# Kernel tuning notes

Hardware: AMD Instinct MI355X
Metric: run time of the kernel (lower is better)

The kernel has to match this reference:

```python
import jax, jax.numpy as jnp
import numpy as np
from math import sqrt


def setup_inputs() -> dict:
    key0 = jax.random.key(0)
    ks = jax.random.split(key0, 7)
    N, H, E, D, S = 32, 16, 128, 128, 2047
    return {
        "query": jax.random.normal(ks[0], (N, H, E), dtype=jnp.float32),
        "key": jax.random.normal(ks[1], (N, H, E), dtype=jnp.float32),
        "value": jax.random.normal(ks[2], (N, H, D), dtype=jnp.float32),
        "keys_cache": jax.random.normal(ks[3], (N, H, S, E), dtype=jnp.float32),
        "values_cache": jax.random.normal(ks[4], (N, H, S, D), dtype=jnp.float32),
        "w_pre": jax.random.normal(ks[5], (H, H), dtype=jnp.float32) * (1.0 / sqrt(H)),
        "w_post": jax.random.normal(ks[6], (H, H), dtype=jnp.float32) * (1.0 / sqrt(H)),
    }


def reference(query, key, value, keys_cache, values_cache, w_pre, w_post):
    # Single recurrent decode step with talking-heads mixing (dropout in eval mode).
    N, H, E = query.shape
    softmax_temp = 1.0 / sqrt(E)
    # Append current key/value to the cache: [N,H,S+1,E] / [N,H,S+1,D]
    keys = jnp.concatenate([keys_cache, key[:, :, None, :]], axis=2)
    values = jnp.concatenate([values_cache, value[:, :, None, :]], axis=2)
    # Scores: [N,H,S]
    QK = jnp.einsum('nhe,nhse->nhs', query, keys)
    # Pre-softmax talking heads (1x1 conv over head axis): out_g = sum_h w[g,h] * in_h
    QK = jnp.einsum('gh,nhs->ngs', w_pre, QK)
    A = jax.nn.softmax(softmax_temp * QK, axis=-1)
    # Post-softmax talking heads
    A = jnp.einsum('gh,nhs->ngs', w_post, A)
    # Weighted value readout: [N,H,D]
    V = jnp.einsum('nhs,nhsd->nhd', A, values)
    return V, keys, values
```

## Files before the change

### kernel.cpp

```cpp
#include <hip/hip_runtime.h>
#include <cstddef>

constexpr int N_  = 32;
constexpr int H_  = 16;
constexpr int E_  = 128;
constexpr int D_  = 128;
constexpr int S_  = 2047;
constexpr int SP1 = 2048;
constexpr int NH  = N_ * H_;

constexpr int ROWS_PER_BLOCK = 256;
constexpr int CHUNKS = SP1 / ROWS_PER_BLOCK;

typedef float vfloat4 __attribute__((ext_vector_type(4)));

__global__ __launch_bounds__(256) void k1_keys_scores(
    const float* __restrict__ query, const float* __restrict__ key,
    const float* __restrict__ keys_cache,
    float* __restrict__ keys_out, float* __restrict__ scores)
{
  __shared__ float sc[ROWS_PER_BLOCK];
  const int bid   = blockIdx.x;
  const int nh    = bid / CHUNKS;
  const int chunk = bid % CHUNKS;
  const int tid   = threadIdx.x;
  const int wave  = tid >> 6;
  const int lane  = tid & 63;
  const int half  = lane >> 5;
  const int lcol  = lane & 31;

  const vfloat4 q4 = *reinterpret_cast<const vfloat4*>(query + (size_t)nh * E_ + lcol * 4);

  #pragma unroll 8
  for (int it = 0; it < ROWS_PER_BLOCK / 8; ++it) {
    const int r = it * 8 + wave * 2 + half;
    const int s = chunk * ROWS_PER_BLOCK + r;
    const float* src = (s < S_) ? (keys_cache + ((size_t)nh * S_ + s) * E_)
                                : (key + (size_t)nh * E_);
    vfloat4 k4 = *reinterpret_cast<const vfloat4*>(src + lcol * 4);
    __builtin_nontemporal_store(k4,
        reinterpret_cast<vfloat4*>(keys_out + ((size_t)nh * SP1 + s) * E_ + lcol * 4));

    float p = q4.x * k4.x + q4.y * k4.y + q4.z * k4.z + q4.w * k4.w;
    p += __shfl_xor(p, 1);
    p += __shfl_xor(p, 2);
    p += __shfl_xor(p, 4);
    p += __shfl_xor(p, 8);
    p += __shfl_xor(p, 16);
    if (lcol == 0) sc[r] = p;
  }
  __syncthreads();
  scores[(size_t)nh * SP1 + chunk * ROWS_PER_BLOCK + tid] = sc[tid];
}

__global__ __launch_bounds__(512) void k2_mix_softmax(
    const float* __restrict__ w_pre, const float* __restrict__ scores,
    float* __restrict__ a_out)
{
  __shared__ float wl[H_];
  __shared__ float redmax[8];
  __shared__ float redsum[8];
  const int n = blockIdx.x >> 4;
  const int g = blockIdx.x & 15;
  const int tid = threadIdx.x;
  const int wave = tid >> 6;
  const int lane = tid & 63;
  const float temp = 0.08838834764831845f;

  if (tid < H_) wl[tid] = w_pre[g * H_ + tid];
  __syncthreads();

  const float* base = scores + (size_t)n * H_ * SP1 + tid * 4;
  float a0 = 0.0f, a1 = 0.0f, a2 = 0.0f, a3 = 0.0f;
  #pragma unroll
  for (int h = 0; h < H_; ++h) {
    vfloat4 v = *reinterpret_cast<const vfloat4*>(base + (size_t)h * SP1);
    const float w = wl[h];
    a0 += w * v.x; a1 += w * v.y; a2 += w * v.z; a3 += w * v.w;
  }
  a0 *= temp; a1 *= temp; a2 *= temp; a3 *= temp;

  float lmax = fmaxf(fmaxf(a0, a1), fmaxf(a2, a3));
  #pragma unroll
  for (int m = 1; m <= 32; m <<= 1) lmax = fmaxf(lmax, __shfl_xor(lmax, m));
  if (lane == 0) redmax[wave] = lmax;
  __syncthreads();
  float bmax = redmax[0];
  #pragma unroll
  for (int w = 1; w < 8; ++w) bmax = fmaxf(bmax, redmax[w]);

  a0 = __expf(a0 - bmax); a1 = __expf(a1 - bmax);
  a2 = __expf(a2 - bmax); a3 = __expf(a3 - bmax);
  float lsum = a0 + a1 + a2 + a3;
  #pragma unroll
  for (int m = 1; m <= 32; m <<= 1) lsum += __shfl_xor(lsum, m);
  if (lane == 0) redsum[wave] = lsum;
  __syncthreads();
  float tot = 0.0f;
  #pragma unroll
  for (int w = 0; w < 8; ++w) tot += redsum[w];
  const float inv = 1.0f / tot;

  vfloat4 o = {a0 * inv, a1 * inv, a2 * inv, a3 * inv};
  *reinterpret_cast<vfloat4*>(a_out + (size_t)(n * H_ + g) * SP1 + tid * 4) = o;
}

__global__ __launch_bounds__(256) void k3_values(
    const float* __restrict__ value, const float* __restrict__ values_cache,
    const float* __restrict__ a, const float* __restrict__ w_post,
    float* __restrict__ values_out, float* __restrict__ partials)
{
  __shared__ float lds[8][128];
  __shared__ float a2[ROWS_PER_BLOCK];
  const int bid   = blockIdx.x;
  const int nh    = bid / CHUNKS;
  const int chunk = bid % CHUNKS;
  const int tid   = threadIdx.x;
  const int wave  = tid >> 6;
  const int lane  = tid & 63;
  const int half  = lane >> 5;
  const int lcol  = lane & 31;
  const int group = wave * 2 + half;

  {
    const int n = nh >> 4;
    const int g = nh & 15;
    const int s = chunk * ROWS_PER_BLOCK + tid;
    const float* abase = a + (size_t)n * H_ * SP1 + s;
    const float* wrow  = w_post + g * H_;
    float acc = 0.0f;
    #pragma unroll
    for (int h = 0; h < H_; ++h) acc += wrow[h] * abase[(size_t)h * SP1];
    a2[tid] = acc;
  }
  __syncthreads();

  float accx = 0.0f, accy = 0.0f, accz = 0.0f, accw = 0.0f;

  #pragma unroll 8
  for (int it = 0; it < ROWS_PER_BLOCK / 8; ++it) {
    const int r = it * 8 + wave * 2 + half;
    const int s = chunk * ROWS_PER_BLOCK + r;
    const float* src = (s < S_) ? (values_cache + ((size_t)nh * S_ + s) * D_)
                                : (value + (size_t)nh * D_);
    vfloat4 v4 = *reinterpret_cast<const vfloat4*>(src + lcol * 4);
    __builtin_nontemporal_store(v4,
        reinterpret_cast<vfloat4*>(values_out + ((size_t)nh * SP1 + s) * D_ + lcol * 4));

    const float w = a2[r];
    accx += w * v4.x;
    accy += w * v4.y;
    accz += w * v4.z;
    accw += w * v4.w;
  }

  lds[group][lcol * 4 + 0] = accx;
  lds[group][lcol * 4 + 1] = accy;
  lds[group][lcol * 4 + 2] = accz;
  lds[group][lcol * 4 + 3] = accw;
  __syncthreads();
  if (tid < 128) {
    float sum = 0.0f;
    #pragma unroll
    for (int gq = 0; gq < 8; ++gq) sum += lds[gq][tid];
    partials[(size_t)bid * 128 + tid] = sum;
  }
}

__global__ __launch_bounds__(256) void k4_reduce(
    const float* __restrict__ partials, float* __restrict__ v_out)
{
  const int g = blockIdx.x * 256 + threadIdx.x;
  const int nh = g >> 7;
  const int d = g & 127;
  float s = 0.0f;
  #pragma unroll
  for (int c = 0; c < CHUNKS; ++c)
    s += partials[((size_t)(nh * CHUNKS + c)) * 128 + d];
  v_out[g] = s;
}

extern "C" void kernel_launch(void* const* d_in, const int* in_sizes, int n_in,
                              void* d_out, int out_size, void* d_ws, size_t ws_size,
                              hipStream_t stream) {
  const float* query        = (const float*)d_in[0];
  const float* key          = (const float*)d_in[1];
  const float* value        = (const float*)d_in[2];
  const float* keys_cache   = (const float*)d_in[3];
  const float* values_cache = (const float*)d_in[4];
  const float* w_pre        = (const float*)d_in[5];
  const float* w_post       = (const float*)d_in[6];

  float* out = (float*)d_out;
  float* v_out      = out;
  float* keys_out   = out + (size_t)NH * D_;
  float* values_out = keys_out + (size_t)NH * SP1 * E_;

  float* buf0     = (float*)d_ws;
  float* buf1     = buf0 + (size_t)NH * SP1;
  float* partials = buf1 + (size_t)NH * SP1;

  k1_keys_scores<<<NH * CHUNKS, 256, 0, stream>>>(query, key, keys_cache,
                                                  keys_out, buf0);
  k2_mix_softmax<<<NH, 512, 0, stream>>>(w_pre, buf0, buf1);
  k3_values<<<NH * CHUNKS, 256, 0, stream>>>(value, values_cache, buf1, w_post,
                                             values_out, partials);
  k4_reduce<<<(NH * 128) / 256, 256, 0, stream>>>(partials, v_out);
}
```

Baseline: 436.9 us.

## Split softmax into blockwise stats pass and fused pre/post head-mixing pass

Replaces the per-(n,g) mix+softmax kernel with two kernels over (n, column chunk). The first computes the pre-mix scores for all 16 heads at once and writes per-block max and sum. The second merges those stats online, recomputes the mix, normalizes, and applies the post-softmax head mixing so k3 only loads a precomputed weight. This removes the 16x redundant score reads per batch and the 16-way gather in k3. The cost is an extra launch, recomputing the pre-mix, and heavy register use from the 16-wide arrays.

```diff
diff --git a/kernel.cpp b/kernel.cpp
--- a/kernel.cpp
+++ b/kernel.cpp
@@ -11,6 +11,7 @@
 
 constexpr int ROWS_PER_BLOCK = 256;
 constexpr int CHUNKS = SP1 / ROWS_PER_BLOCK;
+constexpr int COLCH  = SP1 / 256;
 
 typedef float vfloat4 __attribute__((ext_vector_type(4)));
 
@@ -53,62 +54,127 @@
   scores[(size_t)nh * SP1 + chunk * ROWS_PER_BLOCK + tid] = sc[tid];
 }
 
-__global__ __launch_bounds__(512) void k2_mix_softmax(
-    const float* __restrict__ w_pre, const float* __restrict__ scores,
-    float* __restrict__ a_out)
-{
-  __shared__ float wl[H_];
-  __shared__ float redmax[8];
-  __shared__ float redsum[8];
-  const int n = blockIdx.x >> 4;
-  const int g = blockIdx.x & 15;
+__global__ __launch_bounds__(256) void k2a_stats(
+    const float* __restrict__ scores, const float* __restrict__ w_pre,
+    float* __restrict__ blkstats)
+{
+  __shared__ float wp[H_ * H_];
+  __shared__ float red[4][H_];
+  __shared__ float bmax[H_];
+  const int n   = blockIdx.x >> 3;
+  const int cc  = blockIdx.x & 7;
   const int tid = threadIdx.x;
   const int wave = tid >> 6;
   const int lane = tid & 63;
   const float temp = 0.08838834764831845f;
 
-  if (tid < H_) wl[tid] = w_pre[g * H_ + tid];
-  __syncthreads();
-
-  const float* base = scores + (size_t)n * H_ * SP1 + tid * 4;
-  float a0 = 0.0f, a1 = 0.0f, a2 = 0.0f, a3 = 0.0f;
+  wp[tid] = w_pre[tid];
+  __syncthreads();
+
+  const float* base = scores + (size_t)n * H_ * SP1 + cc * 256 + tid;
+  float sc[H_];
+  #pragma unroll
+  for (int h = 0; h < H_; ++h) sc[h] = base[(size_t)h * SP1];
+
+  float mx[H_];
+  #pragma unroll
+  for (int g = 0; g < H_; ++g) {
+    float acc = 0.0f;
+    #pragma unroll
+    for (int h = 0; h < H_; ++h) acc += wp[g * H_ + h] * sc[h];
+    mx[g] = acc * temp;
+  }
+
+  #pragma unroll
+  for (int g = 0; g < H_; ++g) {
+    float v = mx[g];
+    #pragma unroll
+    for (int m = 1; m <= 32; m <<= 1) v = fmaxf(v, __shfl_xor(v, m));
+    if (lane == 0) red[wave][g] = v;
+  }
+  __syncthreads();
+  if (tid < H_) {
+    float v = fmaxf(fmaxf(red[0][tid], red[1][tid]), fmaxf(red[2][tid], red[3][tid]));
+    bmax[tid] = v;
+    blkstats[((size_t)(n * COLCH + cc) * 2 + 0) * H_ + tid] = v;
+  }
+  __syncthreads();
+
+  #pragma unroll
+  for (int g = 0; g < H_; ++g) {
+    float e = __expf(mx[g] - bmax[g]);
+    #pragma unroll
+    for (int m = 1; m <= 32; m <<= 1) e += __shfl_xor(e, m);
+    if (lane == 0) red[wave][g] = e;
+  }
+  __syncthreads();
+  if (tid < H_) {
+    blkstats[((size_t)(n * COLCH + cc) * 2 + 1) * H_ + tid] =
+        red[0][tid] + red[1][tid] + red[2][tid] + red[3][tid];
+  }
+}
+
+__global__ __launch_bounds__(256) void k2c_a2(
+    const float* __restrict__ scores, const float* __restrict__ blkstats,
+    const float* __restrict__ w_pre, const float* __restrict__ w_post,
+    float* __restrict__ a2out)
+{
+  __shared__ float wp[H_ * H_];
+  __shared__ float wq[H_ * H_];
+  __shared__ float mg[H_];
+  __shared__ float ig[H_];
+  const int n   = blockIdx.x >> 3;
+  const int cc  = blockIdx.x & 7;
+  const int tid = threadIdx.x;
+  const float temp = 0.08838834764831845f;
+
+  wp[tid] = w_pre[tid];
+  wq[tid] = w_post[tid];
+  if (tid < H_) {
+    float bm[COLCH], bs[COLCH];
+    #pragma unroll
+    for (int c = 0; c < COLCH; ++c) {
+      bm[c] = blkstats[((size_t)(n * COLCH + c) * 2 + 0) * H_ + tid];
+      bs[c] = blkstats[((size_t)(n * COLCH + c) * 2 + 1) * H_ + tid];
+    }
+    float m = bm[0];
+    #pragma unroll
+    for (int c = 1; c < COLCH; ++c) m = fmaxf(m, bm[c]);
+    float den = 0.0f;
+    #pragma unroll
+    for (int c = 0; c < COLCH; ++c) den += bs[c] * __expf(bm[c] - m);
+    mg[tid] = m;
+    ig[tid] = 1.0f / den;
+  }
+  __syncthreads();
+
+  const float* base = scores + (size_t)n * H_ * SP1 + cc * 256 + tid;
+  float sc[H_];
+  #pragma unroll
+  for (int h = 0; h < H_; ++h) sc[h] = base[(size_t)h * SP1];
+
+  float P[H_];
   #pragma unroll
   for (int h = 0; h < H_; ++h) {
-    vfloat4 v = *reinterpret_cast<const vfloat4*>(base + (size_t)h * SP1);
-    const float w = wl[h];
-    a0 += w * v.x; a1 += w * v.y; a2 += w * v.z; a3 += w * v.w;
-  }
-  a0 *= temp; a1 *= temp; a2 *= temp; a3 *= temp;
-
-  float lmax = fmaxf(fmaxf(a0, a1), fmaxf(a2, a3));
-  #pragma unroll
-  for (int m = 1; m <= 32; m <<= 1) lmax = fmaxf(lmax, __shfl_xor(lmax, m));
-  if (lane == 0) redmax[wave] = lmax;
-  __syncthreads();
-  float bmax = redmax[0];
-  #pragma unroll
-  for (int w = 1; w < 8; ++w) bmax = fmaxf(bmax, redmax[w]);
-
-  a0 = __expf(a0 - bmax); a1 = __expf(a1 - bmax);
-  a2 = __expf(a2 - bmax); a3 = __expf(a3 - bmax);
-  float lsum = a0 + a1 + a2 + a3;
-  #pragma unroll
-  for (int m = 1; m <= 32; m <<= 1) lsum += __shfl_xor(lsum, m);
-  if (lane == 0) redsum[wave] = lsum;
-  __syncthreads();
-  float tot = 0.0f;
-  #pragma unroll
-  for (int w = 0; w < 8; ++w) tot += redsum[w];
-  const float inv = 1.0f / tot;
-
-  vfloat4 o = {a0 * inv, a1 * inv, a2 * inv, a3 * inv};
-  *reinterpret_cast<vfloat4*>(a_out + (size_t)(n * H_ + g) * SP1 + tid * 4) = o;
+    float acc = 0.0f;
+    #pragma unroll
+    for (int h2 = 0; h2 < H_; ++h2) acc += wp[h * H_ + h2] * sc[h2];
+    P[h] = __expf(acc * temp - mg[h]) * ig[h];
+  }
+
+  #pragma unroll
+  for (int g = 0; g < H_; ++g) {
+    float a = 0.0f;
+    #pragma unroll
+    for (int h = 0; h < H_; ++h) a += wq[g * H_ + h] * P[h];
+    a2out[((size_t)(n * H_ + g)) * SP1 + cc * 256 + tid] = a;
+  }
 }
 
 __global__ __launch_bounds__(256) void k3_values(
     const float* __restrict__ value, const float* __restrict__ values_cache,
-    const float* __restrict__ a, const float* __restrict__ w_post,
-    float* __restrict__ values_out, float* __restrict__ partials)
+    const float* __restrict__ a2buf, float* __restrict__ values_out,
+    float* __restrict__ partials)
 {
   __shared__ float lds[8][128];
   __shared__ float a2[ROWS_PER_BLOCK];
@@ -122,17 +188,7 @@
   const int lcol  = lane & 31;
   const int group = wave * 2 + half;
 
-  {
-    const int n = nh >> 4;
-    const int g = nh & 15;
-    const int s = chunk * ROWS_PER_BLOCK + tid;
-    const float* abase = a + (size_t)n * H_ * SP1 + s;
-    const float* wrow  = w_post + g * H_;
-    float acc = 0.0f;
-    #pragma unroll
-    for (int h = 0; h < H_; ++h) acc += wrow[h] * abase[(size_t)h * SP1];
-    a2[tid] = acc;
-  }
+  a2[tid] = a2buf[(size_t)nh * SP1 + chunk * ROWS_PER_BLOCK + tid];
   __syncthreads();
 
   float accx = 0.0f, accy = 0.0f, accz = 0.0f, accw = 0.0f;
@@ -197,13 +253,15 @@
   float* values_out = keys_out + (size_t)NH * SP1 * E_;
 
   float* buf0     = (float*)d_ws;
-  float* buf1     = buf0 + (size_t)NH * SP1;
-  float* partials = buf1 + (size_t)NH * SP1;
+  float* a2buf    = buf0 + (size_t)NH * SP1;
+  float* blkstats = a2buf + (size_t)NH * SP1;
+  float* partials = blkstats + (size_t)N_ * COLCH * 2 * H_;
 
   k1_keys_scores<<<NH * CHUNKS, 256, 0, stream>>>(query, key, keys_cache,
                                                   keys_out, buf0);
-  k2_mix_softmax<<<NH, 512, 0, stream>>>(w_pre, buf0, buf1);
-  k3_values<<<NH * CHUNKS, 256, 0, stream>>>(value, values_cache, buf1, w_post,
+  k2a_stats<<<N_ * COLCH, 256, 0, stream>>>(buf0, w_pre, blkstats);
+  k2c_a2<<<N_ * COLCH, 256, 0, stream>>>(buf0, blkstats, w_pre, w_post, a2buf);
+  k3_values<<<NH * CHUNKS, 256, 0, stream>>>(value, values_cache, a2buf,
                                              values_out, partials);
   k4_reduce<<<(NH * 128) / 256, 256, 0, stream>>>(partials, v_out);
 }
```

New measurement: 446.3 us. 2.2% more time.
